# Kernel optimization log

Measured on AMD Instinct MI355X. Metric: run time of the kernel, lower is better.

The kernel has to match this reference:

```python
import jax, jax.numpy as jnp
import numpy as np

SCALE = 64 ** -0.5
MAX_LR = 0.01


def newtonschulz5(t, steps=5, eps=1e-7, coefs=(3.4445, -4.775, 2.0315)):
    # t: [h, i, j]; orthogonalize via quintic Newton-Schulz iteration
    a, b, c = coefs
    should_transpose = t.shape[-2] > t.shape[-1]
    if should_transpose:
        t = jnp.swapaxes(t, -1, -2)
    norm = jnp.sqrt(jnp.sum(t * t, axis=(-1, -2), keepdims=True))
    t = t / jnp.maximum(norm, eps)
    for _ in range(steps):
        A = t @ jnp.swapaxes(t, -1, -2)
        B = b * A + c * (A @ A)
        t = a * t + B @ t
    if should_transpose:
        t = jnp.swapaxes(t, -1, -2)
    return t


def setup_inputs() -> dict:
    key = jax.random.key(0)
    ks = jax.random.split(key, 7)
    b, n, d, h, dh = 2, 2048, 512, 8, 64
    s = 0.05  # scale random weights for numerical sanity (softmax not one-hot)
    return {
        "tokens": jax.random.normal(ks[0], (b, n, d), jnp.float32),
        "rms_weight": jnp.ones((d,), jnp.float32),
        "wq": jax.random.normal(ks[1], (h, d, dh), jnp.float32) * s,
        "wk": jax.random.normal(ks[2], (h, d, dh), jnp.float32) * s,
        "wv": jax.random.normal(ks[3], (h, d, dh), jnp.float32) * s,
        "wo": jax.random.normal(ks[4], (h, dh, d), jnp.float32) * s,
        "lr_w": jax.random.normal(ks[5], (1, d), jnp.float32) * s,
        "tv_w": jax.random.normal(ks[6], (d, d), jnp.float32) * s,
        "return_next_memories": 1,
    }


def reference(tokens, rms_weight, wq, wk, wv, wo, lr_w, tv_w, return_next_memories):
    eps = jnp.finfo(tokens.dtype).eps
    # RMSNorm (torch nn.RMSNorm with eps=None -> finfo eps)
    t = tokens * jax.lax.rsqrt(jnp.mean(tokens * tokens, axis=-1, keepdims=True) + eps) * rms_weight

    q = jnp.einsum('bnd,hde->bhne', t, wq)  # [b,h,n,dh]
    k = jnp.einsum('bnd,hde->bhne', t, wk)
    v = jnp.einsum('bnd,hde->bhne', t, wv)

    score = jnp.einsum('bhie,bhje->bhij', q, k) * SCALE
    n = score.shape[-1]
    causal_mask = jnp.triu(jnp.ones((n, n), bool), 1)
    score = jnp.where(causal_mask, -jnp.finfo(score.dtype).max, score)
    attn = jax.nn.softmax(score, axis=-1)
    out = jnp.einsum('bhij,bhje->bhie', attn, v)  # [b,h,n,dh]
    pred_values = jnp.einsum('bhne,hed->bnd', out, wo)

    if not return_next_memories:
        return pred_values

    # target values: Linear(dim,dim,no bias) + LayerNorm(no affine) on shifted tokens
    tv = jnp.einsum('bnd,od->bno', t[:, 1:], tv_w)
    mu = jnp.mean(tv, axis=-1, keepdims=True)
    var = jnp.var(tv, axis=-1, keepdims=True)
    target_values = (tv - mu) * jax.lax.rsqrt(var + 1e-5)

    tok = t[:, :-1]                       # [b,n-1,d]
    pred_fw = pred_values[:, :-1]
    out_t = out[:, :, :-1]
    attn_t = attn[:, :, :-1, :-1]
    q_t, k_t, v_t = q[:, :, :-1], k[:, :, :-1], v[:, :, :-1]

    lr = jax.nn.sigmoid(jnp.einsum('bnd,od->bno', tok, lr_w)) * MAX_LR  # [b,n-1,1]
    error = (target_values - pred_fw) * lr

    dout = jnp.einsum('bnd,hed->bhne', error, wo)            # [b,h,n-1,dh]
    dwo = jnp.einsum('bnd,bhne->hed', error, out_t)          # [h,dh,d]
    delta = jnp.sum(dout * out_t, axis=-1, keepdims=True)    # [b,h,n-1,1]
    dv = jnp.einsum('bhij,bhie->bhje', attn_t, dout)
    dattn = jnp.einsum('bhje,bhie->bhij', v_t, dout)
    dscore = SCALE * attn_t * (dattn - delta)
    dq = jnp.einsum('bhje,bhij->bhie', k_t, dscore)
    dk = jnp.einsum('bhie,bhij->bhje', q_t, dscore)
    dwq = jnp.einsum('bhie,bid->hde', dq, tok)
    dwk = jnp.einsum('bhje,bjd->hde', dk, tok)
    dwv = jnp.einsum('bhje,bjd->hde', dv, tok)

    # muon update: Newton-Schulz orthogonalization of value/output fast-weight grads
    dwv = newtonschulz5(dwv)
    dwo = newtonschulz5(dwo)

    return (pred_values, dwq, dwk, dwv, dwo)
```

## Files before the change

kernel.cpp:

```cpp
#include <hip/hip_runtime.h>
#include <float.h>
#include <math.h>

#define B_   2
#define N_   2048
#define D_   512
#define H_   8
#define DH_  64
#define NM_  2047
#define SCALE_F 0.125f
#define LBK 72

typedef __attribute__((ext_vector_type(8))) short bf16x8;
typedef __attribute__((ext_vector_type(4))) float f32x4;
#define MFMA_B16(a,b,c) __builtin_amdgcn_mfma_f32_16x16x32_bf16(a,b,c,0,0,0)

__device__ __forceinline__ short f2bf(float f){
  unsigned u = __float_as_uint(f);
  unsigned r = u + 0x7fffu + ((u>>16)&1u);
  return (short)(r>>16);
}
__device__ __forceinline__ float bf2f(short s){
  return __uint_as_float(((unsigned)(unsigned short)s)<<16);
}
__device__ __forceinline__ void lds_fence(){
  asm volatile("s_waitcnt lgkmcnt(0)" ::: "memory");
  __builtin_amdgcn_sched_barrier(0);
}
__device__ __forceinline__ void tload(const short* __restrict__ src, size_t stride,
                                      int tid, int4& r0, int4& r1){
  int rr = tid>>2, cc = (tid&3)<<4;
  r0 = *(const int4*)&src[(size_t)rr*stride + cc];
  r1 = *(const int4*)&src[(size_t)rr*stride + cc + 8];
}
__device__ __forceinline__ void twrite(short (*dst)[LBK], int tid,
                                       const int4& r0, const int4& r1){
  int rr = tid>>2, cc = (tid&3)<<4;
  *(int4*)&dst[rr][cc]   = r0;
  *(int4*)&dst[rr][cc+8] = r1;
}
__device__ __forceinline__ float wred64(float v){
  #pragma unroll
  for(int off=32; off; off>>=1) v += __shfl_down(v, off, 64);
  return v;
}

__device__ __forceinline__ void gemm64(const short* __restrict__ A, size_t lda,
    const short* __restrict__ Bt, size_t ldb, int nk,
    short (*as)[LBK], short (*bs)[LBK], f32x4* acc){
  int tid=threadIdx.x, w=tid>>6, lane=tid&63, lg=lane>>4, ln=lane&15;
  int4 a0,a1,b0,b1;
  tload(A, lda, tid, a0,a1);
  tload(Bt, ldb, tid, b0,b1);
  for(int kt=0;kt<nk;++kt){
    __syncthreads();
    twrite(as, tid, a0,a1);
    twrite(bs, tid, b0,b1);
    if(kt+1<nk){
      tload(A +(size_t)(kt+1)*64, lda, tid, a0,a1);
      tload(Bt+(size_t)(kt+1)*64, ldb, tid, b0,b1);
    }
    __syncthreads();
    __builtin_amdgcn_s_setprio(1);
    #pragma unroll
    for(int s=0;s<2;s++){
      bf16x8 a = *(const bf16x8*)&as[w*16+ln][32*s+lg*8];
      #pragma unroll
      for(int nb=0;nb<4;nb++){
        bf16x8 b = *(const bf16x8*)&bs[nb*16+ln][32*s+lg*8];
        acc[nb]=MFMA_B16(a,b,acc[nb]);
      }
    }
    __builtin_amdgcn_s_setprio(0);
  }
}

__global__ __launch_bounds__(256) void k_rmsnorm(const float* __restrict__ tok,
    const float* __restrict__ w, short* __restrict__ tb){
  int row = blockIdx.x;
  int tid = threadIdx.x;
  if(row>=4096){ tb[(size_t)row*D_+tid]=0; tb[(size_t)row*D_+tid+256]=0; return; }
  const float* x = tok + (size_t)row*D_;
  float v0 = x[tid], v1 = x[tid+256];
  float s = v0*v0 + v1*v1;
  s = wred64(s);
  __shared__ float red[4];
  if((tid&63)==0) red[tid>>6] = s;
  __syncthreads();
  float tot = red[0]+red[1]+red[2]+red[3];
  float sc = rsqrtf(tot*(1.f/512.f) + 1.1920929e-7f);
  tb[(size_t)row*D_+tid]     = f2bf(v0*sc*w[tid]);
  tb[(size_t)row*D_+tid+256] = f2bf(v1*sc*w[tid+256]);
}

__global__ __launch_bounds__(256) void k_wprep(const float* __restrict__ wq,
    const float* __restrict__ wk, const float* __restrict__ wv,
    const float* __restrict__ wo, const float* __restrict__ tvw,
    short* __restrict__ wqt, short* __restrict__ wkt, short* __restrict__ wvt,
    short* __restrict__ wob, short* __restrict__ wot, short* __restrict__ tvwb){
  __shared__ short l[64][66];
  int bx=blockIdx.x, tid=threadIdx.x;
  if(bx<192){
    const float* w = (bx<64)? wq : (bx<128)? wk : wv;
    short* wt      = (bx<64)? wqt: (bx<128)? wkt: wvt;
    int lb=bx&63, h=lb>>3, d0=(lb&7)*64;
    for(int kk=0;kk<16;kk++){
      int idx=kk*256+tid, rr=idx>>6, cc=idx&63;
      l[cc][rr] = f2bf(w[((size_t)h*512 + d0+rr)*64 + cc]);
    }
    __syncthreads();
    for(int kk=0;kk<16;kk++){
      int idx=kk*256+tid, rr=idx>>6, cc=idx&63;
      wt[((size_t)h*64+rr)*512 + d0+cc] = l[rr][cc];
    }
  } else if(bx<256){
    int lb=bx-192, r0=(lb>>3)*64, c0=(lb&7)*64;
    for(int kk=0;kk<16;kk++){
      int idx=kk*256+tid, rr=idx>>6, cc=idx&63;
      l[cc][rr] = f2bf(wo[(size_t)(r0+rr)*512 + c0+cc]);
    }
    __syncthreads();
    for(int kk=0;kk<16;kk++){
      int idx=kk*256+tid, rr=idx>>6, cc=idx&63;
      wot[(size_t)(c0+rr)*512 + r0+cc] = l[rr][cc];
    }
  } else if(bx<264){
    size_t base=(size_t)(bx-256)*32768;
    for(int kk=0;kk<128;kk++) wob[base+kk*256+tid]=f2bf(wo[base+kk*256+tid]);
  } else {
    size_t base=(size_t)(bx-264)*32768;
    for(int kk=0;kk<128;kk++) tvwb[base+kk*256+tid]=f2bf(tvw[base+kk*256+tid]);
  }
}

__global__ __launch_bounds__(256) void k_trans_b(const short* __restrict__ in,
    short* __restrict__ outt){
  __shared__ short l[64][66];
  int r0=blockIdx.x<<6, c0=blockIdx.y<<6, tid=threadIdx.x;
  for(int kk=0;kk<16;kk++){
    int idx=kk*256+tid, rr=idx>>6, cc=idx&63;
    l[cc][rr]=in[(size_t)(r0+rr)*512 + c0+cc];
  }
  __syncthreads();
  for(int kk=0;kk<16;kk++){
    int idx=kk*256+tid, rr=idx>>6, cc=idx&63;
    outt[(size_t)(c0+rr)*4096 + r0+cc]=l[rr][cc];
  }
}
__global__ __launch_bounds__(256) void k_trans_f(const float* __restrict__ in,
    short* __restrict__ outn, short* __restrict__ outt){
  __shared__ short l[64][66];
  int r0=blockIdx.x<<6, c0=blockIdx.y<<6, tid=threadIdx.x;
  for(int kk=0;kk<16;kk++){
    int idx=kk*256+tid, rr=idx>>6, cc=idx&63;
    short v=f2bf(in[(size_t)(r0+rr)*512 + c0+cc]);
    outn[(size_t)(r0+rr)*512 + c0+cc]=v;
    l[cc][rr]=v;
  }
  __syncthreads();
  for(int kk=0;kk<16;kk++){
    int idx=kk*256+tid, rr=idx>>6, cc=idx&63;
    outt[(size_t)(c0+rr)*4096 + r0+cc]=l[rr][cc];
  }
}

__global__ __launch_bounds__(256) void k_gemm_qkv(const short* __restrict__ tb,
    const short* __restrict__ wqt, const short* __restrict__ wkt, const short* __restrict__ wvt,
    short* __restrict__ qh, short* __restrict__ kh, short* __restrict__ vh,
    short* __restrict__ qt, short* __restrict__ kt, short* __restrict__ vt){
  __shared__ __attribute__((aligned(16))) short as[64][LBK], bs[64][LBK];
  int r0=blockIdx.x<<6, ct=blockIdx.y, which=ct>>3, h=ct&7;
  const short* Bt=(which==0?wqt:which==1?wkt:wvt)+(size_t)h*32768;
  f32x4 acc[4];
  #pragma unroll
  for(int nb=0;nb<4;nb++) acc[nb]=(f32x4){0.f,0.f,0.f,0.f};
  gemm64(tb+(size_t)r0*512, 512, Bt, 512, 8, as, bs, acc);
  short* on=(which==0?qh:which==1?kh:vh);
  short* ot=(which==0?qt:which==1?kt:vt);
  int tid=threadIdx.x, w=tid>>6, lane=tid&63, lg=lane>>4, ln=lane&15;
  size_t bh=(size_t)(r0>>11)*8+h;
  int n0=(r0&2047)+w*16+lg*4;
  #pragma unroll
  for(int nb=0;nb<4;nb++){
    int e=nb*16+ln;
    short4 s4;
    s4.x=f2bf(acc[nb][0]); s4.y=f2bf(acc[nb][1]);
    s4.z=f2bf(acc[nb][2]); s4.w=f2bf(acc[nb][3]);
    on[(bh*2048+n0  )*64+e]=s4.x;
    on[(bh*2048+n0+1)*64+e]=s4.y;
    on[(bh*2048+n0+2)*64+e]=s4.z;
    on[(bh*2048+n0+3)*64+e]=s4.w;
    *(short4*)&ot[(bh*64+e)*2048+n0]=s4;
  }
}

__global__ __launch_bounds__(256) void k_fa_fwd(const short* __restrict__ qh,
    const short* __restrict__ kh, const short* __restrict__ vt,
    float* __restrict__ op0, float* __restrict__ op1, float* __restrict__ mlb){
  int bh = blockIdx.x, qq = blockIdx.y, half = blockIdx.z;
  int it = (qq<16)? (31-qq) : (qq-16);
  int i0 = it<<6;
  const short* qhb = qh + (size_t)bh*N_*DH_;
  const short* khb = kh + (size_t)bh*N_*DH_;
  const short* vtb = vt + (size_t)bh*DH_*N_;
  __shared__ __attribute__((aligned(16))) short ks[64][LBK], vts[64][LBK];
  __shared__ __attribute__((aligned(16))) short psb[4][16][LBK];
  int tid=threadIdx.x, w=tid>>6, lane=tid&63, lg=lane>>4, ln=lane&15;
  bf16x8 aq[2];
  #pragma unroll
  for(int s=0;s<2;s++)
    aq[s] = *(const bf16x8*)&qhb[(size_t)(i0+w*16+ln)*DH_ + 32*s + lg*8];
  f32x4 acc[4];
  float mrow[4], lrow[4];
  #pragma unroll
  for(int nb=0;nb<4;nb++) acc[nb]=(f32x4){0.f,0.f,0.f,0.f};
  #pragma unroll
  for(int r=0;r<4;r++){ mrow[r]=-FLT_MAX; lrow[r]=0.f; }
  int4 ka0,ka1,va0,va1;
  tload(khb+(size_t)half*64*DH_, DH_, tid, ka0,ka1);
  tload(vtb+half*64, N_, tid, va0,va1);
  for(int jt=half;jt<=it;jt+=2){
    int j0 = jt<<6;
    __syncthreads();
    twrite(ks, tid, ka0,ka1);
    twrite(vts, tid, va0,va1);
    if(jt+2<=it){
      tload(khb+(size_t)(jt+2)*64*DH_, DH_, tid, ka0,ka1);
      tload(vtb+(jt+2)*64, N_, tid, va0,va1);
    }
    __syncthreads();
    f32x4 sv[4];
    __builtin_amdgcn_s_setprio(1);
    #pragma unroll
    for(int nb=0;nb<4;nb++){
      f32x4 z = {0.f,0.f,0.f,0.f};
      #pragma unroll
      for(int s=0;s<2;s++){
        bf16x8 bk = *(const bf16x8*)&ks[nb*16+ln][32*s + lg*8];
        z = MFMA_B16(aq[s], bk, z);
      }
      sv[nb]=z;
    }
    __builtin_amdgcn_s_setprio(0);
    int iiB = i0 + w*16 + lg*4;
    #pragma unroll
    for(int r=0;r<4;r++){
      int ii = iiB + r;
      float srow[4]; float mx = -FLT_MAX;
      #pragma unroll
      for(int nb=0;nb<4;nb++){
        float x = sv[nb][r]*SCALE_F;
        if(j0+nb*16+ln > ii) x = -FLT_MAX;
        srow[nb]=x; mx=fmaxf(mx,x);
      }
      mx=fmaxf(mx,__shfl_xor(mx,1)); mx=fmaxf(mx,__shfl_xor(mx,2));
      mx=fmaxf(mx,__shfl_xor(mx,4)); mx=fmaxf(mx,__shfl_xor(mx,8));
      float mn = fmaxf(mrow[r], mx);
      float rs = 0.f;
      #pragma unroll
      for(int nb=0;nb<4;nb++){
        float pv = __expf(srow[nb]-mn);
        psb[w][lg*4+r][ln+16*nb]=f2bf(pv); rs+=pv;
      }
      rs+=__shfl_xor(rs,1); rs+=__shfl_xor(rs,2);
      rs+=__shfl_xor(rs,4); rs+=__shfl_xor(rs,8);
      float corr = __expf(mrow[r]-mn);
      lrow[r]=lrow[r]*corr+rs; mrow[r]=mn;
      #pragma unroll
      for(int nb=0;nb<4;nb++) acc[nb][r]*=corr;
    }
    lds_fence();
    __builtin_amdgcn_s_setprio(1);
    #pragma unroll
    for(int nb=0;nb<4;nb++){
      #pragma unroll
      for(int s=0;s<2;s++){
        bf16x8 pa = *(const bf16x8*)&psb[w][ln][32*s + lg*8];
        bf16x8 bv = *(const bf16x8*)&vts[nb*16+ln][32*s + lg*8];
        acc[nb] = MFMA_B16(pa, bv, acc[nb]);
      }
    }
    __builtin_amdgcn_s_setprio(0);
    lds_fence();
  }
  float* op   = half? op1 : op0;
  float* marr = mlb + half*65536;
  float* larr = marr + 32768;
  #pragma unroll
  for(int r=0;r<4;r++){
    int ii = i0 + w*16 + lg*4 + r;
    size_t row = (size_t)bh*2048 + ii;
    #pragma unroll
    for(int nb=0;nb<4;nb++)
      op[row*64 + nb*16+ln] = acc[nb][r];
    if(ln==0){ marr[row]=mrow[r]; larr[row]=lrow[r]; }
  }
}

__global__ __launch_bounds__(256) void k_fa_merge(const float* __restrict__ op0,
    const float* __restrict__ op1, const float* __restrict__ mlb,
    short* __restrict__ obb, float* __restrict__ lse){
  int row = blockIdx.x*4 + (threadIdx.x>>6);
  int lane = threadIdx.x&63;
  float m0 = mlb[row],        l0 = mlb[32768+row];
  float m1 = mlb[65536+row],  l1 = mlb[98304+row];
  float m  = fmaxf(m0,m1);
  float c0 = __expf(m0-m), c1 = __expf(m1-m);
  float l  = l0*c0 + l1*c1;
  float o  = (op0[(size_t)row*64+lane]*c0 + op1[(size_t)row*64+lane]*c1)/l;
  int bh = row>>11, i = row&2047, b = bh>>3, h = bh&7;
  obb[((size_t)(b*2048+i))*512 + h*64 + lane] = f2bf(o);
  if(lane==0) lse[row] = m + logf(l);
}

__global__ __launch_bounds__(256) void k_gemm_pred(const short* __restrict__ obb,
    const short* __restrict__ wot, float* __restrict__ pred){
  __shared__ __attribute__((aligned(16))) short as[64][LBK], bs[64][LBK];
  int r0=blockIdx.x<<6, c0=blockIdx.y<<6;
  f32x4 acc[4];
  #pragma unroll
  for(int nb=0;nb<4;nb++) acc[nb]=(f32x4){0.f,0.f,0.f,0.f};
  gemm64(obb+(size_t)r0*512, 512, wot+(size_t)c0*512, 512, 8, as, bs, acc);
  int tid=threadIdx.x, w=tid>>6, lane=tid&63, lg=lane>>4, ln=lane&15;
  int row=r0+w*16+lg*4;
  #pragma unroll
  for(int nb=0;nb<4;nb++)
    #pragma unroll
    for(int r=0;r<4;r++)
      pred[(size_t)(row+r)*512 + c0+nb*16+ln]=acc[nb][r];
}

__global__ __launch_bounds__(256) void k_gemm_tv(const short* __restrict__ tb,
    const short* __restrict__ tvwb, float* __restrict__ er){
  __shared__ __attribute__((aligned(16))) short as[64][LBK], bs[64][LBK];
  int r0=blockIdx.x<<6, c0=blockIdx.y<<6;
  f32x4 acc[4];
  #pragma unroll
  for(int nb=0;nb<4;nb++) acc[nb]=(f32x4){0.f,0.f,0.f,0.f};
  gemm64(tb+(size_t)(r0+1)*512, 512, tvwb+(size_t)c0*512, 512, 8, as, bs, acc);
  int tid=threadIdx.x, w=tid>>6, lane=tid&63, lg=lane>>4, ln=lane&15;
  int row=r0+w*16+lg*4;
  #pragma unroll
  for(int nb=0;nb<4;nb++)
    #pragma unroll
    for(int r=0;r<4;r++){
      float v=(((row+r)&2047)==2047)?0.f:acc[nb][r];
      er[(size_t)(row+r)*512 + c0+nb*16+ln]=v;
    }
}

__global__ __launch_bounds__(256) void k_lnerr(float* __restrict__ er,
    const short* __restrict__ tb, const float* __restrict__ pred,
    const float* __restrict__ lrw){
  int kr = blockIdx.x;
  int b = kr/NM_, n = kr-b*NM_;
  size_t row=(size_t)b*2048+n;
  float* tv = er + row*512;
  const short* tok = tb + row*512;
  const float* pr  = pred + row*512;
  int tid=threadIdx.x;
  float v0=tv[tid], v1=tv[tid+256];
  float s1=v0+v1, s2=v0*v0+v1*v1;
  float s3=bf2f(tok[tid])*lrw[tid] + bf2f(tok[tid+256])*lrw[tid+256];
  s1=wred64(s1); s2=wred64(s2); s3=wred64(s3);
  __shared__ float r1[4],r2[4],r3[4];
  if((tid&63)==0){ int w=tid>>6; r1[w]=s1; r2[w]=s2; r3[w]=s3; }
  __syncthreads();
  float S1=r1[0]+r1[1]+r1[2]+r1[3];
  float S2=r2[0]+r2[1]+r2[2]+r2[3];
  float S3=r3[0]+r3[1]+r3[2]+r3[3];
  float mu  = S1*(1.f/512.f);
  float var = S2*(1.f/512.f) - mu*mu;
  float rstd= rsqrtf(var + 1e-5f);
  float lr  = 0.01f/(1.f+__expf(-S3));
  tv[tid]     = ((v0-mu)*rstd - pr[tid])*lr;
  tv[tid+256] = ((v1-mu)*rstd - pr[tid+256])*lr;
}

__global__ __launch_bounds__(256) void k_gemm_dout(const short* __restrict__ erb,
    const short* __restrict__ wob, short* __restrict__ doh, short* __restrict__ dot){
  __shared__ __attribute__((aligned(16))) short as[64][LBK], bs[64][LBK];
  int r0=blockIdx.x<<6, h=blockIdx.y;
  f32x4 acc[4];
  #pragma unroll
  for(int nb=0;nb<4;nb++) acc[nb]=(f32x4){0.f,0.f,0.f,0.f};
  gemm64(erb+(size_t)r0*512, 512, wob+(size_t)h*32768, 512, 8, as, bs, acc);
  int tid=threadIdx.x, w=tid>>6, lane=tid&63, lg=lane>>4, ln=lane&15;
  size_t bh=(size_t)(r0>>11)*8+h;
  int n0=(r0&2047)+w*16+lg*4;
  #pragma unroll
  for(int nb=0;nb<4;nb++){
    int e=nb*16+ln;
    short4 s4;
    s4.x=f2bf(acc[nb][0]); s4.y=f2bf(acc[nb][1]);
    s4.z=f2bf(acc[nb][2]); s4.w=f2bf(acc[nb][3]);
    doh[(bh*2048+n0  )*64+e]=s4.x;
    doh[(bh*2048+n0+1)*64+e]=s4.y;
    doh[(bh*2048+n0+2)*64+e]=s4.z;
    doh[(bh*2048+n0+3)*64+e]=s4.w;
    *(short4*)&dot[(bh*64+e)*2048+n0]=s4;
  }
}

__global__ __launch_bounds__(256) void k_delta(const short* __restrict__ doh,
    const short* __restrict__ obb, float* __restrict__ delta){
  int rid = blockIdx.x*4 + (threadIdx.x>>6);
  int lane = threadIdx.x&63;
  if(rid >= B_*H_*NM_) return;
  int b = rid/(H_*NM_); int rem = rid - b*H_*NM_;
  int h = rem/NM_; int i = rem - h*NM_;
  float v = bf2f(doh[((size_t)(b*H_+h)*N_ + i)*DH_ + lane])
          * bf2f(obb[((size_t)(b*N_+i))*D_ + h*DH_ + lane]);
  v = wred64(v);
  if(lane==0) delta[((size_t)(b*H_+h))*N_ + i] = v;
}

__global__ __launch_bounds__(256) void k_fa_dq(const short* __restrict__ qh,
    const short* __restrict__ kh, const short* __restrict__ vh,
    const short* __restrict__ kt, const short* __restrict__ doh,
    const float* __restrict__ lse, const float* __restrict__ delta,
    short* __restrict__ dqt, short* __restrict__ dqp1){
  int bh = blockIdx.x, it = blockIdx.y, half = blockIdx.z;
  int i0 = it<<6;
  const short* qhb = qh + (size_t)bh*N_*DH_;
  const short* khb = kh + (size_t)bh*N_*DH_;
  const short* vhb = vh + (size_t)bh*N_*DH_;
  const short* ktb = kt + (size_t)bh*DH_*N_;
  const short* dohb= doh+ (size_t)bh*N_*DH_;
  __shared__ __attribute__((aligned(16))) short ks[64][LBK], vs[64][LBK], kts[64][LBK];
  __shared__ __attribute__((aligned(16))) short psb[4][16][LBK];
  int tid=threadIdx.x, w=tid>>6, lane=tid&63, lg=lane>>4, ln=lane&15;
  bf16x8 aq[2], ad[2];
  float Lr[4], dl[4];
  #pragma unroll
  for(int s=0;s<2;s++){
    aq[s]=*(const bf16x8*)&qhb[(size_t)(i0+w*16+ln)*DH_+32*s+lg*8];
    ad[s]=*(const bf16x8*)&dohb[(size_t)(i0+w*16+ln)*DH_+32*s+lg*8];
  }
  #pragma unroll
  for(int r=0;r<4;r++){
    int ii=i0+w*16+lg*4+r;
    Lr[r]=lse[(size_t)bh*N_+ii];
    dl[r]=(ii<NM_)?delta[(size_t)bh*N_+ii]:0.f;
  }
  f32x4 acc[4];
  #pragma unroll
  for(int nb=0;nb<4;nb++) acc[nb]=(f32x4){0.f,0.f,0.f,0.f};
  int4 ka0,ka1,va0,va1,ta0,ta1;
  tload(khb+(size_t)half*64*DH_, DH_, tid, ka0,ka1);
  tload(vhb+(size_t)half*64*DH_, DH_, tid, va0,va1);
  tload(ktb+half*64, N_, tid, ta0,ta1);
  for(int jt=half;jt<=it;jt+=2){
    int j0=jt<<6;
    __syncthreads();
    twrite(ks, tid, ka0,ka1);
    twrite(vs, tid, va0,va1);
    twrite(kts, tid, ta0,ta1);
    if(jt+2<=it){
      tload(khb+(size_t)(jt+2)*64*DH_, DH_, tid, ka0,ka1);
      tload(vhb+(size_t)(jt+2)*64*DH_, DH_, tid, va0,va1);
      tload(ktb+(jt+2)*64, N_, tid, ta0,ta1);
    }
    __syncthreads();
    f32x4 sv[4], dav[4];
    __builtin_amdgcn_s_setprio(1);
    #pragma unroll
    for(int nb=0;nb<4;nb++){
      f32x4 z={0.f,0.f,0.f,0.f}, zd={0.f,0.f,0.f,0.f};
      #pragma unroll
      for(int s=0;s<2;s++){
        bf16x8 bk=*(const bf16x8*)&ks[nb*16+ln][32*s+lg*8];
        bf16x8 bv=*(const bf16x8*)&vs[nb*16+ln][32*s+lg*8];
        z = MFMA_B16(aq[s], bk, z);
        zd= MFMA_B16(ad[s], bv, zd);
      }
      sv[nb]=z; dav[nb]=zd;
    }
    __builtin_amdgcn_s_setprio(0);
    #pragma unroll
    for(int r=0;r<4;r++){
      int ii=i0+w*16+lg*4+r;
      #pragma unroll
      for(int nb=0;nb<4;nb++){
        int jj=j0+nb*16+ln;
        float pv=__expf(sv[nb][r]*SCALE_F - Lr[r]);
        float dsv=SCALE_F*pv*(dav[nb][r]-dl[r]);
        if(jj>ii || ii>=NM_ || jj>=NM_) dsv=0.f;
        psb[w][lg*4+r][ln+16*nb]=f2bf(dsv);
      }
    }
    lds_fence();
    __builtin_amdgcn_s_setprio(1);
    #pragma unroll
    for(int nb=0;nb<4;nb++){
      #pragma unroll
      for(int s=0;s<2;s++){
        bf16x8 pa = *(const bf16x8*)&psb[w][ln][32*s+lg*8];
        bf16x8 bk = *(const bf16x8*)&kts[nb*16+ln][32*s+lg*8];
        acc[nb]=MFMA_B16(pa,bk,acc[nb]);
      }
    }
    __builtin_amdgcn_s_setprio(0);
    lds_fence();
  }
  short* dst = half? dqp1 : dqt;
  #pragma unroll
  for(int nb=0;nb<4;nb++){
    short4 s4;
    s4.x=f2bf(acc[nb][0]); s4.y=f2bf(acc[nb][1]);
    s4.z=f2bf(acc[nb][2]); s4.w=f2bf(acc[nb][3]);
    *(short4*)&dst[((size_t)bh*64 + nb*16+ln)*2048 + i0+w*16+lg*4]=s4;
  }
}

__global__ __launch_bounds__(256) void k_dqred(short* __restrict__ dqt,
    const short* __restrict__ dqp1){
  size_t i = ((size_t)blockIdx.x*256 + threadIdx.x)*8;
  int4 a = *(const int4*)&dqt[i];
  int4 b = *(const int4*)&dqp1[i];
  short* pa=(short*)&a; const short* pb=(const short*)&b;
  short out[8];
  #pragma unroll
  for(int k=0;k<8;k++) out[k]=f2bf(bf2f(pa[k])+bf2f(pb[k]));
  *(int4*)&dqt[i] = *(int4*)out;
}

__global__ __launch_bounds__(256) void k_fa_dkv(const short* __restrict__ kh,
    const short* __restrict__ vh, const short* __restrict__ qh,
    const short* __restrict__ qt, const short* __restrict__ doh,
    const short* __restrict__ dot,
    const float* __restrict__ lse, const float* __restrict__ delta,
    short* __restrict__ dkt, short* __restrict__ dvt,
    short* __restrict__ dkp1, short* __restrict__ dvp1){
  int bh = blockIdx.x, jt = blockIdx.y, half = blockIdx.z;
  int j0 = jt<<6;
  const short* khb = kh + (size_t)bh*N_*DH_;
  const short* vhb = vh + (size_t)bh*N_*DH_;
  const short* qhb = qh + (size_t)bh*N_*DH_;
  const short* qtb = qt + (size_t)bh*DH_*N_;
  const short* dohb= doh+ (size_t)bh*N_*DH_;
  const short* dotb= dot+ (size_t)bh*DH_*N_;
  __shared__ __attribute__((aligned(16))) short qs[64][LBK], dos[64][LBK], qts[64][LBK], dots[64][LBK];
  __shared__ __attribute__((aligned(16))) short psv[4][16][LBK], psk[4][16][LBK];
  __shared__ float Ls[64], dls[64];
  int tid=threadIdx.x, w=tid>>6, lane=tid&63, lg=lane>>4, ln=lane&15;
  bf16x8 akf[2], avf[2];
  #pragma unroll
  for(int s=0;s<2;s++){
    akf[s]=*(const bf16x8*)&khb[(size_t)(j0+w*16+ln)*DH_+32*s+lg*8];
    avf[s]=*(const bf16x8*)&vhb[(size_t)(j0+w*16+ln)*DH_+32*s+lg*8];
  }
  f32x4 accv[4], acck[4];
  #pragma unroll
  for(int nb=0;nb<4;nb++){
    accv[nb]=(f32x4){0.f,0.f,0.f,0.f};
    acck[nb]=(f32x4){0.f,0.f,0.f,0.f};
  }
  int it0 = jt + half;
  int4 qa0,qa1,da0,da1,qta0,qta1,dta0,dta1;
  float Lnx=0.f, dlnx=0.f;
  {
    int ip = (it0<32)? (it0<<6) : 0;
    tload(qhb+(size_t)ip*DH_, DH_, tid, qa0,qa1);
    tload(dohb+(size_t)ip*DH_, DH_, tid, da0,da1);
    tload(qtb+ip, N_, tid, qta0,qta1);
    tload(dotb+ip, N_, tid, dta0,dta1);
    if(tid<64){
      int ii=ip+tid;
      Lnx=lse[(size_t)bh*N_+ii];
      dlnx=(ii<NM_)?delta[(size_t)bh*N_+ii]:0.f;
    }
  }
  for(int it=it0; it<32; it+=2){
    int i0=it<<6;
    __syncthreads();
    twrite(qs, tid, qa0,qa1);
    twrite(dos, tid, da0,da1);
    twrite(qts, tid, qta0,qta1);
    twrite(dots, tid, dta0,dta1);
    if(tid<64){ Ls[tid]=Lnx; dls[tid]=dlnx; }
    if(it+2<32){
      int i1=(it+2)<<6;
      tload(qhb+(size_t)i1*DH_, DH_, tid, qa0,qa1);
      tload(dohb+(size_t)i1*DH_, DH_, tid, da0,da1);
      tload(qtb+i1, N_, tid, qta0,qta1);
      tload(dotb+i1, N_, tid, dta0,dta1);
      if(tid<64){
        int ii=i1+tid;
        Lnx=lse[(size_t)bh*N_+ii];
        dlnx=(ii<NM_)?delta[(size_t)bh*N_+ii]:0.f;
      }
    }
    __syncthreads();
    f32x4 sv[4], dav[4];
    __builtin_amdgcn_s_setprio(1);
    #pragma unroll
    for(int nb=0;nb<4;nb++){
      f32x4 z={0.f,0.f,0.f,0.f}, zd={0.f,0.f,0.f,0.f};
      #pragma unroll
      for(int s=0;s<2;s++){
        bf16x8 bq=*(const bf16x8*)&qs[nb*16+ln][32*s+lg*8];
        bf16x8 bd=*(const bf16x8*)&dos[nb*16+ln][32*s+lg*8];
        z = MFMA_B16(akf[s], bq, z);
        zd= MFMA_B16(avf[s], bd, zd);
      }
      sv[nb]=z; dav[nb]=zd;
    }
    __builtin_amdgcn_s_setprio(0);
    #pragma unroll
    for(int nb=0;nb<4;nb++){
      float Lc=Ls[nb*16+ln], dlc=dls[nb*16+ln];
      int ii=i0+nb*16+ln;
      #pragma unroll
      for(int r=0;r<4;r++){
        int jj=j0+w*16+lg*4+r;
        float pv=__expf(sv[nb][r]*SCALE_F - Lc);
        bool msk=(jj>ii)||(ii>=NM_)||(jj>=NM_);
        if(msk) pv=0.f;
        float ds = msk?0.f: SCALE_F*pv*(dav[nb][r]-dlc);
        psv[w][lg*4+r][ln+16*nb]=f2bf(pv);
        psk[w][lg*4+r][ln+16*nb]=f2bf(ds);
      }
    }
    lds_fence();
    __builtin_amdgcn_s_setprio(1);
    #pragma unroll
    for(int nb=0;nb<4;nb++){
      #pragma unroll
      for(int s=0;s<2;s++){
        bf16x8 pa = *(const bf16x8*)&psv[w][ln][32*s+lg*8];
        bf16x8 bd = *(const bf16x8*)&dots[nb*16+ln][32*s+lg*8];
        accv[nb]=MFMA_B16(pa,bd,accv[nb]);
        bf16x8 pk = *(const bf16x8*)&psk[w][ln][32*s+lg*8];
        bf16x8 bq = *(const bf16x8*)&qts[nb*16+ln][32*s+lg*8];
        acck[nb]=MFMA_B16(pk,bq,acck[nb]);
      }
    }
    __builtin_amdgcn_s_setprio(0);
    lds_fence();
  }
  short* dvd = half? dvp1 : dvt;
  short* dkd = half? dkp1 : dkt;
  #pragma unroll
  for(int nb=0;nb<4;nb++){
    int e=nb*16+ln, n0=j0+w*16+lg*4;
    short4 s4;
    s4.x=f2bf(accv[nb][0]); s4.y=f2bf(accv[nb][1]);
    s4.z=f2bf(accv[nb][2]); s4.w=f2bf(accv[nb][3]);
    *(short4*)&dvd[((size_t)bh*64+e)*2048 + n0]=s4;
    s4.x=f2bf(acck[nb][0]); s4.y=f2bf(acck[nb][1]);
    s4.z=f2bf(acck[nb][2]); s4.w=f2bf(acck[nb][3]);
    *(short4*)&dkd[((size_t)bh*64+e)*2048 + n0]=s4;
  }
}

__global__ __launch_bounds__(256) void k_dkvred(short* __restrict__ dkt,
    short* __restrict__ dvt, const short* __restrict__ dkp1,
    const short* __restrict__ dvp1){
  int bid = blockIdx.x;
  short* dst; const short* src;
  if(bid<1024){ dst=dkt; src=dkp1; } else { dst=dvt; src=dvp1; bid-=1024; }
  size_t i = ((size_t)bid*256 + threadIdx.x)*8;
  int4 a = *(const int4*)&dst[i];
  int4 b = *(const int4*)&src[i];
  short* pa=(short*)&a; const short* pb=(const short*)&b;
  short out[8];
  #pragma unroll
  for(int k=0;k<8;k++) out[k]=f2bf(bf2f(pa[k])+bf2f(pb[k]));
  *(int4*)&dst[i] = *(int4*)out;
}

__global__ __launch_bounds__(256) void k_gemm_wgq(const short* __restrict__ tt,
    const short* __restrict__ g, float* __restrict__ par){
  __shared__ __attribute__((aligned(16))) short as[64][LBK], bs[64][LBK];
  int dt=blockIdx.x, h=blockIdx.y, sp=blockIdx.z;
  int b=sp>>2, n0b=(sp&3)*512;
  f32x4 acc[4];
  #pragma unroll
  for(int nb=0;nb<4;nb++) acc[nb]=(f32x4){0.f,0.f,0.f,0.f};
  gemm64(tt + (size_t)(dt*64)*4096 + sp*512, 4096,
         g  + ((size_t)(b*8+h)*64)*2048 + n0b, 2048, 8, as, bs, acc);
  int tid=threadIdx.x, w=tid>>6, lane=tid&63, lg=lane>>4, ln=lane&15;
  int row=w*16+lg*4;
  #pragma unroll
  for(int nb=0;nb<4;nb++)
    #pragma unroll
    for(int r=0;r<4;r++)
      par[(size_t)sp*262144 + (size_t)h*32768 + (size_t)(dt*64+row+r)*64 + nb*16+ln]=acc[nb][r];
}

__global__ __launch_bounds__(256) void k_gemm_wgo(const short* __restrict__ outt,
    const short* __restrict__ ert, float* __restrict__ par){
  __shared__ __attribute__((aligned(16))) short as[64][LBK], bs[64][LBK];
  int ct=blockIdx.x, h=blockIdx.y, sp=blockIdx.z;
  f32x4 acc[4];
  #pragma unroll
  for(int nb=0;nb<4;nb++) acc[nb]=(f32x4){0.f,0.f,0.f,0.f};
  gemm64(outt + (size_t)(h*64)*4096 + sp*512, 4096,
         ert  + (size_t)(ct*64)*4096 + sp*512, 4096, 8, as, bs, acc);
  int tid=threadIdx.x, w=tid>>6, lane=tid&63, lg=lane>>4, ln=lane&15;
  int row=w*16+lg*4;
  #pragma unroll
  for(int nb=0;nb<4;nb++)
    #pragma unroll
    for(int r=0;r<4;r++)
      par[(size_t)sp*262144 + (size_t)h*32768 + (size_t)(row+r)*512 + ct*64+nb*16+ln]=acc[nb][r];
}

__global__ __launch_bounds__(256) void k_wred_direct(const float* __restrict__ par,
    float* __restrict__ dst){
  int idx = blockIdx.x*256 + threadIdx.x;
  float s=0.f;
  #pragma unroll
  for(int sp=0;sp<8;sp++) s += par[(size_t)sp*262144 + idx];
  dst[idx]=s;
}
__global__ __launch_bounds__(256) void k_wred_xv(const float* __restrict__ par,
    float* __restrict__ X0){
  int idx = blockIdx.x*256 + threadIdx.x;
  float s=0.f;
  #pragma unroll
  for(int sp=0;sp<8;sp++) s += par[(size_t)sp*262144 + idx];
  int h=idx>>15, rem=idx&32767, d=rem>>6, e=rem&63;
  X0[(size_t)h*32768 + (size_t)e*512 + d]=s;
}
__global__ __launch_bounds__(256) void k_wred_xo(const float* __restrict__ par,
    float* __restrict__ X0){
  int idx = blockIdx.x*256 + threadIdx.x;
  float s=0.f;
  #pragma unroll
  for(int sp=0;sp<8;sp++) s += par[(size_t)sp*262144 + idx];
  X0[262144 + idx]=s;
}

__global__ __launch_bounds__(256) void k_ns_fused(const float* __restrict__ X0,
    float* __restrict__ dwv, float* __restrict__ dwo){
  __shared__ __attribute__((aligned(16))) short Xl[64][520];
  __shared__ __attribute__((aligned(16))) short Xt[512][72];
  __shared__ __attribute__((aligned(16))) short Al[64][72];
  __shared__ __attribute__((aligned(16))) short Bl[64][72];
  __shared__ float red[4];
  int m = blockIdx.x, tid=threadIdx.x, w=tid>>6, lane=tid&63, lg=lane>>4, ln=lane&15;
  const float* Xg = X0 + (size_t)m*32768;
  float ss=0.f;
  for(int kk=0;kk<128;kk++){ float v=Xg[kk*256+tid]; ss+=v*v; }
  ss=wred64(ss);
  if(lane==0) red[w]=ss;
  __syncthreads();
  float sc = 1.f/fmaxf(sqrtf(red[0]+red[1]+red[2]+red[3]), 1e-7f);
  for(int kk=0;kk<128;kk++){
    int idx=kk*256+tid; int rr=idx>>9, cc=idx&511;
    short v=f2bf(Xg[idx]*sc);
    Xl[rr][cc]=v; Xt[cc][rr]=v;
  }
  __syncthreads();
  for(int iter=0; iter<5; ++iter){
    f32x4 accA[4];
    #pragma unroll
    for(int nb=0;nb<4;nb++) accA[nb]=(f32x4){0.f,0.f,0.f,0.f};
    for(int kt=0;kt<8;kt++){
      #pragma unroll
      for(int s=0;s<2;s++){
        bf16x8 a = *(const bf16x8*)&Xl[w*16+ln][kt*64+32*s+lg*8];
        #pragma unroll
        for(int nb=0;nb<4;nb++){
          bf16x8 b = *(const bf16x8*)&Xl[nb*16+ln][kt*64+32*s+lg*8];
          accA[nb]=MFMA_B16(a,b,accA[nb]);
        }
      }
    }
    #pragma unroll
    for(int nb=0;nb<4;nb++)
      #pragma unroll
      for(int r=0;r<4;r++)
        Al[w*16+lg*4+r][nb*16+ln]=f2bf(accA[nb][r]);
    __syncthreads();
    f32x4 acc2[4];
    #pragma unroll
    for(int nb=0;nb<4;nb++) acc2[nb]=(f32x4){0.f,0.f,0.f,0.f};
    #pragma unroll
    for(int s=0;s<2;s++){
      bf16x8 a = *(const bf16x8*)&Al[w*16+ln][32*s+lg*8];
      #pragma unroll
      for(int nb=0;nb<4;nb++){
        bf16x8 b = *(const bf16x8*)&Al[nb*16+ln][32*s+lg*8];
        acc2[nb]=MFMA_B16(a,b,acc2[nb]);
      }
    }
    #pragma unroll
    for(int nb=0;nb<4;nb++)
      #pragma unroll
      for(int r=0;r<4;r++)
        Bl[w*16+lg*4+r][nb*16+ln]=f2bf(-4.775f*accA[nb][r] + 2.0315f*acc2[nb][r]);
    __syncthreads();
    #pragma unroll
    for(int ph=0; ph<2; ++ph){
      f32x4 xn[4][4];
      #pragma unroll
      for(int c4=0;c4<4;c4++){
        int ct=ph*4+c4;
        #pragma unroll
        for(int nb=0;nb<4;nb++) xn[c4][nb]=(f32x4){0.f,0.f,0.f,0.f};
        #pragma unroll
        for(int s=0;s<2;s++){
          bf16x8 a = *(const bf16x8*)&Bl[w*16+ln][32*s+lg*8];
          #pragma unroll
          for(int nb=0;nb<4;nb++){
            bf16x8 b = *(const bf16x8*)&Xt[ct*64+nb*16+ln][32*s+lg*8];
            xn[c4][nb]=MFMA_B16(a,b,xn[c4][nb]);
          }
        }
        #pragma unroll
        for(int nb=0;nb<4;nb++)
          #pragma unroll
          for(int r=0;r<4;r++)
            xn[c4][nb][r] += 3.4445f*bf2f(Xl[w*16+lg*4+r][ct*64+nb*16+ln]);
      }
      __syncthreads();
      if(iter<4){
        #pragma unroll
        for(int c4=0;c4<4;c4++){
          int ct=ph*4+c4;
          #pragma unroll
          for(int nb=0;nb<4;nb++){
            int d=ct*64+nb*16+ln, row0=w*16+lg*4;
            short4 s4;
            s4.x=f2bf(xn[c4][nb][0]); s4.y=f2bf(xn[c4][nb][1]);
            s4.z=f2bf(xn[c4][nb][2]); s4.w=f2bf(xn[c4][nb][3]);
            Xl[row0  ][d]=s4.x; Xl[row0+1][d]=s4.y;
            Xl[row0+2][d]=s4.z; Xl[row0+3][d]=s4.w;
            *(short4*)&Xt[d][row0]=s4;
          }
        }
        __syncthreads();
      } else {
        #pragma unroll
        for(int c4=0;c4<4;c4++){
          int ct=ph*4+c4;
          #pragma unroll
          for(int nb=0;nb<4;nb++){
            int d=ct*64+nb*16+ln, row0=w*16+lg*4;
            #pragma unroll
            for(int r=0;r<4;r++){
              float v=xn[c4][nb][r];
              int e=row0+r;
              if(m<8) dwv[(size_t)m*32768 + (size_t)d*64 + e]=v;
              else    dwo[(size_t)(m-8)*32768 + (size_t)e*512 + d]=v;
            }
          }
        }
      }
    }
  }
}

extern "C" void kernel_launch(void* const* d_in, const int* in_sizes, int n_in,
                              void* d_out, int out_size, void* d_ws, size_t ws_size,
                              hipStream_t stream) {
  const float* tokens=(const float*)d_in[0];
  const float* rmsw =(const float*)d_in[1];
  const float* wq   =(const float*)d_in[2];
  const float* wk   =(const float*)d_in[3];
  const float* wv   =(const float*)d_in[4];
  const float* wo   =(const float*)d_in[5];
  const float* lrw  =(const float*)d_in[6];
  const float* tvw  =(const float*)d_in[7];
  float* out = (float*)d_out;
  float* ws  = (float*)d_ws;

  short* tb   = (short*)(ws);
  short* tt   = (short*)(ws + 1064960);
  short* qh   = (short*)(ws + 2113536);
  short* kh   = (short*)(ws + 3162112);
  short* vh   = (short*)(ws + 4210688);
  short* qt   = (short*)(ws + 5259264);
  short* kt   = (short*)(ws + 6307840);
  short* vt   = (short*)(ws + 7356416);
  float* er_  = ws + 8404992;
  float* op0  = ws + 8404992;
  short* dqp1 = (short*)(ws + 8404992);
  short* dkp1 = (short*)(ws + 8404992);
  short* dvp1 = (short*)(ws + 9453568);
  short* obb  = (short*)(ws + 10502144);
  short* outt = (short*)(ws + 11550720);
  short* erb  = (short*)(ws + 12599296);
  short* ert  = (short*)(ws + 13647872);
  short* doh  = (short*)(ws + 14696448);
  short* dot  = (short*)(ws + 15745024);
  float* par_ = ws + 14696448;
  float* op1  = ws + 14696448;
  short* dqt  = (short*)(ws + 16793600);
  float* mlb  = ws + 16793600;
  short* dkt  = (short*)(ws + 17842176);
  short* dvt  = (short*)(ws + 18890752);
  short* wqt  = (short*)(ws + 19939328);
  short* wkt  = (short*)(ws + 20070400);
  short* wvt  = (short*)(ws + 20201472);
  short* wob  = (short*)(ws + 20332544);
  short* wot  = (short*)(ws + 20463616);
  short* tvwb = (short*)(ws + 20594688);
  float* lse_ = ws + 20725760;
  float* dlt_ = ws + 20758528;
  float* X0_  = ws + 20791296;

  float* OUT_PRED = out;
  float* OUT_DWQ  = out + 2097152;
  float* OUT_DWK  = out + 2359296;
  float* OUT_DWV  = out + 2621440;
  float* OUT_DWO  = out + 2883584;

  k_rmsnorm<<<4160,256,0,stream>>>(tokens, rmsw, tb);
  k_wprep<<<272,256,0,stream>>>(wq,wk,wv,wo,tvw, wqt,wkt,wvt,wob,wot,tvwb);
  k_gemm_qkv<<<dim3(64,24),256,0,stream>>>(tb, wqt,wkt,wvt, qh,kh,vh, qt,kt,vt);
  k_fa_fwd<<<dim3(16,32,2),256,0,stream>>>(qh, kh, vt, op0, op1, mlb);
  k_fa_merge<<<8192,256,0,stream>>>(op0, op1, mlb, obb, lse_);
  k_gemm_pred<<<dim3(64,8),256,0,stream>>>(obb, wot, OUT_PRED);

  if(out_size < 3145728) return;

  k_trans_b<<<dim3(64,8),256,0,stream>>>(tb, tt);
  k_gemm_tv<<<dim3(64,8),256,0,stream>>>(tb, tvwb, er_);
  k_lnerr<<<4094,256,0,stream>>>(er_, tb, OUT_PRED, lrw);
  k_trans_f<<<dim3(64,8),256,0,stream>>>(er_, erb, ert);
  k_gemm_dout<<<dim3(64,8),256,0,stream>>>(erb, wob, doh, dot);
  k_delta<<<8188,256,0,stream>>>(doh, obb, dlt_);
  k_fa_dq<<<dim3(16,32,2),256,0,stream>>>(qh, kh, vh, kt, doh, lse_, dlt_, dqt, dqp1);
  k_dqred<<<1024,256,0,stream>>>(dqt, dqp1);
  k_fa_dkv<<<dim3(16,32,2),256,0,stream>>>(kh, vh, qh, qt, doh, dot, lse_, dlt_,
                                           dkt, dvt, dkp1, dvp1);
  k_dkvred<<<2048,256,0,stream>>>(dkt, dvt, dkp1, dvp1);
  k_trans_b<<<dim3(64,8),256,0,stream>>>(obb, outt);

  k_gemm_wgq<<<dim3(8,8,8),256,0,stream>>>(tt, dqt, par_);
  k_wred_direct<<<1024,256,0,stream>>>(par_, OUT_DWQ);
  k_gemm_wgq<<<dim3(8,8,8),256,0,stream>>>(tt, dkt, par_);
  k_wred_direct<<<1024,256,0,stream>>>(par_, OUT_DWK);
  k_gemm_wgq<<<dim3(8,8,8),256,0,stream>>>(tt, dvt, par_);
  k_wred_xv<<<1024,256,0,stream>>>(par_, X0_);
  k_gemm_wgo<<<dim3(8,8,8),256,0,stream>>>(outt, ert, par_);
  k_wred_xo<<<1024,256,0,stream>>>(par_, X0_);

  k_ns_fused<<<16,256,0,stream>>>(X0_, OUT_DWV, OUT_DWO);
}
```

Measured before the change: 318.6 us.

## Skip causal mask on off-diagonal tiles and widen Newton-Schulz kernel to 16 waves

The flash forward, dQ and dK/dV kernels now branch so that off-diagonal key/query tiles skip the per-element causal and boundary masking. Tiles on the diagonal and the last row tile keep the full mask. Separately, the fused Newton-Schulz kernel goes from 256 to 1024 threads per block: each of 16 waves computes a single 16x16 tile of A and B and a 16x128 slice of the update. This is meant to cut the long serial runtime of that 16-block kernel, at the cost of more barriers and higher register and LDS pressure per block.

After: 311.1 us. 1.02x faster.

```diff
diff --git a/kernel.cpp b/kernel.cpp
--- a/kernel.cpp
+++ b/kernel.cpp
@@ -221,6 +221,7 @@
   tload(vtb+half*64, N_, tid, va0,va1);
   for(int jt=half;jt<=it;jt+=2){
     int j0 = jt<<6;
+    bool diag = (jt==it);
     __syncthreads();
     twrite(ks, tid, ka0,ka1);
     twrite(vts, tid, va0,va1);
@@ -247,11 +248,19 @@
     for(int r=0;r<4;r++){
       int ii = iiB + r;
       float srow[4]; float mx = -FLT_MAX;
-      #pragma unroll
-      for(int nb=0;nb<4;nb++){
-        float x = sv[nb][r]*SCALE_F;
-        if(j0+nb*16+ln > ii) x = -FLT_MAX;
-        srow[nb]=x; mx=fmaxf(mx,x);
+      if(diag){
+        #pragma unroll
+        for(int nb=0;nb<4;nb++){
+          float x = sv[nb][r]*SCALE_F;
+          if(j0+nb*16+ln > ii) x = -FLT_MAX;
+          srow[nb]=x; mx=fmaxf(mx,x);
+        }
+      } else {
+        #pragma unroll
+        for(int nb=0;nb<4;nb++){
+          float x = sv[nb][r]*SCALE_F;
+          srow[nb]=x; mx=fmaxf(mx,x);
+        }
       }
       mx=fmaxf(mx,__shfl_xor(mx,1)); mx=fmaxf(mx,__shfl_xor(mx,2));
       mx=fmaxf(mx,__shfl_xor(mx,4)); mx=fmaxf(mx,__shfl_xor(mx,8));
@@ -452,6 +461,7 @@
   tload(ktb+half*64, N_, tid, ta0,ta1);
   for(int jt=half;jt<=it;jt+=2){
     int j0=jt<<6;
+    bool msk_needed = (jt==it) || (it==31);
     __syncthreads();
     twrite(ks, tid, ka0,ka1);
     twrite(vs, tid, va0,va1);
@@ -477,17 +487,27 @@
       sv[nb]=z; dav[nb]=zd;
     }
     __builtin_amdgcn_s_setprio(0);
-    #pragma unroll
-    for(int r=0;r<4;r++){
-      int ii=i0+w*16+lg*4+r;
-      #pragma unroll
-      for(int nb=0;nb<4;nb++){
-        int jj=j0+nb*16+ln;
-        float pv=__expf(sv[nb][r]*SCALE_F - Lr[r]);
-        float dsv=SCALE_F*pv*(dav[nb][r]-dl[r]);
-        if(jj>ii || ii>=NM_ || jj>=NM_) dsv=0.f;
-        psb[w][lg*4+r][ln+16*nb]=f2bf(dsv);
-      }
+    if(msk_needed){
+      #pragma unroll
+      for(int r=0;r<4;r++){
+        int ii=i0+w*16+lg*4+r;
+        #pragma unroll
+        for(int nb=0;nb<4;nb++){
+          int jj=j0+nb*16+ln;
+          float pv=__expf(sv[nb][r]*SCALE_F - Lr[r]);
+          float dsv=SCALE_F*pv*(dav[nb][r]-dl[r]);
+          if(jj>ii || ii>=NM_ || jj>=NM_) dsv=0.f;
+          psb[w][lg*4+r][ln+16*nb]=f2bf(dsv);
+        }
+      }
+    } else {
+      #pragma unroll
+      for(int r=0;r<4;r++)
+        #pragma unroll
+        for(int nb=0;nb<4;nb++){
+          float pv=__expf(sv[nb][r]*SCALE_F - Lr[r]);
+          psb[w][lg*4+r][ln+16*nb]=f2bf(SCALE_F*pv*(dav[nb][r]-dl[r]));
+        }
     }
     lds_fence();
     __builtin_amdgcn_s_setprio(1);
@@ -573,6 +593,7 @@
   }
   for(int it=it0; it<32; it+=2){
     int i0=it<<6;
+    bool msk_needed = (it==jt) || (it==31);
     __syncthreads();
     twrite(qs, tid, qa0,qa1);
     twrite(dos, tid, da0,da1);
@@ -607,19 +628,32 @@
       sv[nb]=z; dav[nb]=zd;
     }
     __builtin_amdgcn_s_setprio(0);
-    #pragma unroll
-    for(int nb=0;nb<4;nb++){
-      float Lc=Ls[nb*16+ln], dlc=dls[nb*16+ln];
-      int ii=i0+nb*16+ln;
-      #pragma unroll
-      for(int r=0;r<4;r++){
-        int jj=j0+w*16+lg*4+r;
-        float pv=__expf(sv[nb][r]*SCALE_F - Lc);
-        bool msk=(jj>ii)||(ii>=NM_)||(jj>=NM_);
-        if(msk) pv=0.f;
-        float ds = msk?0.f: SCALE_F*pv*(dav[nb][r]-dlc);
-        psv[w][lg*4+r][ln+16*nb]=f2bf(pv);
-        psk[w][lg*4+r][ln+16*nb]=f2bf(ds);
+    if(msk_needed){
+      #pragma unroll
+      for(int nb=0;nb<4;nb++){
+        float Lc=Ls[nb*16+ln], dlc=dls[nb*16+ln];
+        int ii=i0+nb*16+ln;
+        #pragma unroll
+        for(int r=0;r<4;r++){
+          int jj=j0+w*16+lg*4+r;
+          float pv=__expf(sv[nb][r]*SCALE_F - Lc);
+          bool msk=(jj>ii)||(ii>=NM_)||(jj>=NM_);
+          if(msk) pv=0.f;
+          float ds = msk?0.f: SCALE_F*pv*(dav[nb][r]-dlc);
+          psv[w][lg*4+r][ln+16*nb]=f2bf(pv);
+          psk[w][lg*4+r][ln+16*nb]=f2bf(ds);
+        }
+      }
+    } else {
+      #pragma unroll
+      for(int nb=0;nb<4;nb++){
+        float Lc=Ls[nb*16+ln], dlc=dls[nb*16+ln];
+        #pragma unroll
+        for(int r=0;r<4;r++){
+          float pv=__expf(sv[nb][r]*SCALE_F - Lc);
+          psv[w][lg*4+r][ln+16*nb]=f2bf(pv);
+          psk[w][lg*4+r][ln+16*nb]=f2bf(SCALE_F*pv*(dav[nb][r]-dlc));
+        }
       }
     }
     lds_fence();
@@ -733,121 +767,91 @@
   X0[262144 + idx]=s;
 }
 
-__global__ __launch_bounds__(256) void k_ns_fused(const float* __restrict__ X0,
+__global__ __launch_bounds__(1024) void k_ns_fused(const float* __restrict__ X0,
     float* __restrict__ dwv, float* __restrict__ dwo){
   __shared__ __attribute__((aligned(16))) short Xl[64][520];
   __shared__ __attribute__((aligned(16))) short Xt[512][72];
   __shared__ __attribute__((aligned(16))) short Al[64][72];
   __shared__ __attribute__((aligned(16))) short Bl[64][72];
-  __shared__ float red[4];
+  __shared__ float red[16];
   int m = blockIdx.x, tid=threadIdx.x, w=tid>>6, lane=tid&63, lg=lane>>4, ln=lane&15;
+  int wr=w>>2, wc=w&3;
   const float* Xg = X0 + (size_t)m*32768;
   float ss=0.f;
-  for(int kk=0;kk<128;kk++){ float v=Xg[kk*256+tid]; ss+=v*v; }
+  for(int kk=0;kk<32;kk++){ float v=Xg[kk*1024+tid]; ss+=v*v; }
   ss=wred64(ss);
   if(lane==0) red[w]=ss;
   __syncthreads();
-  float sc = 1.f/fmaxf(sqrtf(red[0]+red[1]+red[2]+red[3]), 1e-7f);
-  for(int kk=0;kk<128;kk++){
-    int idx=kk*256+tid; int rr=idx>>9, cc=idx&511;
+  float tot=0.f;
+  #pragma unroll
+  for(int i=0;i<16;i++) tot+=red[i];
+  float sc = 1.f/fmaxf(sqrtf(tot), 1e-7f);
+  for(int kk=0;kk<32;kk++){
+    int idx=kk*1024+tid; int rr=idx>>9, cc=idx&511;
     short v=f2bf(Xg[idx]*sc);
     Xl[rr][cc]=v; Xt[cc][rr]=v;
   }
   __syncthreads();
   for(int iter=0; iter<5; ++iter){
-    f32x4 accA[4];
-    #pragma unroll
-    for(int nb=0;nb<4;nb++) accA[nb]=(f32x4){0.f,0.f,0.f,0.f};
-    for(int kt=0;kt<8;kt++){
+    f32x4 accA=(f32x4){0.f,0.f,0.f,0.f};
+    #pragma unroll
+    for(int kt=0;kt<16;kt++){
+      bf16x8 a = *(const bf16x8*)&Xl[wr*16+ln][kt*32+lg*8];
+      bf16x8 b = *(const bf16x8*)&Xl[wc*16+ln][kt*32+lg*8];
+      accA=MFMA_B16(a,b,accA);
+    }
+    #pragma unroll
+    for(int r=0;r<4;r++) Al[wr*16+lg*4+r][wc*16+ln]=f2bf(accA[r]);
+    __syncthreads();
+    f32x4 acc2=(f32x4){0.f,0.f,0.f,0.f};
+    #pragma unroll
+    for(int s=0;s<2;s++){
+      bf16x8 a = *(const bf16x8*)&Al[wr*16+ln][32*s+lg*8];
+      bf16x8 b = *(const bf16x8*)&Al[wc*16+ln][32*s+lg*8];
+      acc2=MFMA_B16(a,b,acc2);
+    }
+    #pragma unroll
+    for(int r=0;r<4;r++)
+      Bl[wr*16+lg*4+r][wc*16+ln]=f2bf(-4.775f*accA[r] + 2.0315f*acc2[r]);
+    __syncthreads();
+    int rg=(w&3)<<4, cg=(w>>2)<<7;
+    f32x4 xn[8];
+    #pragma unroll
+    for(int nb=0;nb<8;nb++){
+      xn[nb]=(f32x4){0.f,0.f,0.f,0.f};
       #pragma unroll
       for(int s=0;s<2;s++){
-        bf16x8 a = *(const bf16x8*)&Xl[w*16+ln][kt*64+32*s+lg*8];
+        bf16x8 a = *(const bf16x8*)&Bl[rg+ln][32*s+lg*8];
+        bf16x8 b = *(const bf16x8*)&Xt[cg+nb*16+ln][32*s+lg*8];
+        xn[nb]=MFMA_B16(a,b,xn[nb]);
+      }
+      #pragma unroll
+      for(int r=0;r<4;r++)
+        xn[nb][r] += 3.4445f*bf2f(Xl[rg+lg*4+r][cg+nb*16+ln]);
+    }
+    __syncthreads();
+    if(iter<4){
+      #pragma unroll
+      for(int nb=0;nb<8;nb++){
+        int d=cg+nb*16+ln, row0=rg+lg*4;
+        short4 s4;
+        s4.x=f2bf(xn[nb][0]); s4.y=f2bf(xn[nb][1]);
+        s4.z=f2bf(xn[nb][2]); s4.w=f2bf(xn[nb][3]);
+        Xl[row0  ][d]=s4.x; Xl[row0+1][d]=s4.y;
+        Xl[row0+2][d]=s4.z; Xl[row0+3][d]=s4.w;
+        *(short4*)&Xt[d][row0]=s4;
+      }
+      __syncthreads();
+    } else {
+      #pragma unroll
+      for(int nb=0;nb<8;nb++){
+        int d=cg+nb*16+ln, row0=rg+lg*4;
         #pragma unroll
-        for(int nb=0;nb<4;nb++){
-          bf16x8 b = *(const bf16x8*)&Xl[nb*16+ln][kt*64+32*s+lg*8];
-          accA[nb]=MFMA_B16(a,b,accA[nb]);
-        }
-      }
-    }
-    #pragma unroll
-    for(int nb=0;nb<4;nb++)
-      #pragma unroll
-      for(int r=0;r<4;r++)
-        Al[w*16+lg*4+r][nb*16+ln]=f2bf(accA[nb][r]);
-    __syncthreads();
-    f32x4 acc2[4];
-    #pragma unroll
-    for(int nb=0;nb<4;nb++) acc2[nb]=(f32x4){0.f,0.f,0.f,0.f};
-    #pragma unroll
-    for(int s=0;s<2;s++){
-      bf16x8 a = *(const bf16x8*)&Al[w*16+ln][32*s+lg*8];
-      #pragma unroll
-      for(int nb=0;nb<4;nb++){
-        bf16x8 b = *(const bf16x8*)&Al[nb*16+ln][32*s+lg*8];
-        acc2[nb]=MFMA_B16(a,b,acc2[nb]);
-      }
-    }
-    #pragma unroll
-    for(int nb=0;nb<4;nb++)
-      #pragma unroll
-      for(int r=0;r<4;r++)
-        Bl[w*16+lg*4+r][nb*16+ln]=f2bf(-4.775f*accA[nb][r] + 2.0315f*acc2[nb][r]);
-    __syncthreads();
-    #pragma unroll
-    for(int ph=0; ph<2; ++ph){
-      f32x4 xn[4][4];
-      #pragma unroll
-      for(int c4=0;c4<4;c4++){
-        int ct=ph*4+c4;
-        #pragma unroll
-        for(int nb=0;nb<4;nb++) xn[c4][nb]=(f32x4){0.f,0.f,0.f,0.f};
-        #pragma unroll
-        for(int s=0;s<2;s++){
-          bf16x8 a = *(const bf16x8*)&Bl[w*16+ln][32*s+lg*8];
-          #pragma unroll
-          for(int nb=0;nb<4;nb++){
-            bf16x8 b = *(const bf16x8*)&Xt[ct*64+nb*16+ln][32*s+lg*8];
-            xn[c4][nb]=MFMA_B16(a,b,xn[c4][nb]);
-          }
-        }
-        #pragma unroll
-        for(int nb=0;nb<4;nb++)
-          #pragma unroll
-          for(int r=0;r<4;r++)
-            xn[c4][nb][r] += 3.4445f*bf2f(Xl[w*16+lg*4+r][ct*64+nb*16+ln]);
-      }
-      __syncthreads();
-      if(iter<4){
-        #pragma unroll
-        for(int c4=0;c4<4;c4++){
-          int ct=ph*4+c4;
-          #pragma unroll
-          for(int nb=0;nb<4;nb++){
-            int d=ct*64+nb*16+ln, row0=w*16+lg*4;
-            short4 s4;
-            s4.x=f2bf(xn[c4][nb][0]); s4.y=f2bf(xn[c4][nb][1]);
-            s4.z=f2bf(xn[c4][nb][2]); s4.w=f2bf(xn[c4][nb][3]);
-            Xl[row0  ][d]=s4.x; Xl[row0+1][d]=s4.y;
-            Xl[row0+2][d]=s4.z; Xl[row0+3][d]=s4.w;
-            *(short4*)&Xt[d][row0]=s4;
-          }
-        }
-        __syncthreads();
-      } else {
-        #pragma unroll
-        for(int c4=0;c4<4;c4++){
-          int ct=ph*4+c4;
-          #pragma unroll
-          for(int nb=0;nb<4;nb++){
-            int d=ct*64+nb*16+ln, row0=w*16+lg*4;
-            #pragma unroll
-            for(int r=0;r<4;r++){
-              float v=xn[c4][nb][r];
-              int e=row0+r;
-              if(m<8) dwv[(size_t)m*32768 + (size_t)d*64 + e]=v;
-              else    dwo[(size_t)(m-8)*32768 + (size_t)e*512 + d]=v;
-            }
-          }
+        for(int r=0;r<4;r++){
+          float v=xn[nb][r];
+          int e=row0+r;
+          if(m<8) dwv[(size_t)m*32768 + (size_t)d*64 + e]=v;
+          else    dwo[(size_t)(m-8)*32768 + (size_t)e*512 + d]=v;
         }
       }
     }
@@ -940,5 +944,5 @@
   k_gemm_wgo<<<dim3(8,8,8),256,0,stream>>>(outt, ert, par_);
   k_wred_xo<<<1024,256,0,stream>>>(par_, X0_);
 
-  k_ns_fused<<<16,256,0,stream>>>(X0_, OUT_DWV, OUT_DWO);
-}
+  k_ns_fused<<<16,1024,0,stream>>>(X0_, OUT_DWV, OUT_DWO);
+}
```
